# Kernel optimization log

Measured on AMD Instinct MI355X. Metric: run time of the kernel, lower is better.

Reference implementation:

```python
import jax, jax.numpy as jnp
import numpy as np

EPS = 1e-12

def _pairwise_dist(a, b):
    # a: [B,N,3], b: [B,M,3] -> Euclidean distances [B,N,M]
    d2 = (jnp.sum(a * a, -1)[:, :, None]
          + jnp.sum(b * b, -1)[:, None, :]
          - 2.0 * jnp.einsum('bnd,bmd->bnm', a, b))
    return jnp.sqrt(jnp.maximum(d2, EPS))


def setup_inputs() -> dict:
    key = jax.random.key(0)
    k1, k2, k3 = jax.random.split(key, 3)
    B, N, M = 16, 4096, 1024
    shape_xyz = jax.random.normal(k1, (B, N, 6), dtype=jnp.float32)
    skel_xyz = jax.random.normal(k2, (B, M, 3), dtype=jnp.float32)
    skel_nori = jax.random.normal(k3, (B, M, 3), dtype=jnp.float32)
    return {"shape_xyz": shape_xyz, "skel_xyz": skel_xyz, "skel_nori": skel_nori}


def reference(shape_xyz, skel_xyz, skel_nori):
    normal = shape_xyz[:, :, 3:6]          # [B,N,3]
    pts = shape_xyz[:, :, :3]              # [B,N,3]
    B = skel_nori.shape[0]

    # Chamfer-style closest distances (sum of min Euclidean distances, both ways)
    d_shape2skel = _pairwise_dist(pts, skel_xyz)   # [B,N,M]
    cd1 = jnp.sum(jnp.min(d_shape2skel, axis=2))
    cd2 = jnp.sum(jnp.min(d_shape2skel, axis=1))   # same matrix transposed
    loss_cd = (cd1 + cd2) * 0.0001

    # KNN (k=2) of each skeletal point among shape points (cKDTree equivalent)
    d_skel2shape = jnp.transpose(d_shape2skel, (0, 2, 1))  # [B,M,N]
    _, idx = jax.lax.top_k(-d_skel2shape, 2)               # [B,M,2]

    # Gather normals of the 2 nearest shape points: [B,M,2,3]
    knn_normals = jnp.take_along_axis(normal[:, None, :, :],
                                      idx[:, :, :, None], axis=2)
    dots = jnp.einsum('bmd,bmkd->bmk', skel_nori, knn_normals)  # [B,M,2]
    # |dot| averaged over k, summed over (b, j), divided by batch size
    loss_normal = jnp.sum(jnp.mean(jnp.abs(dots), axis=-1)) / B

    return loss_cd + 0.001 * loss_normal
```

## Files before the change

### kernel.cpp

```cpp
#include <hip/hip_runtime.h>
#include <cfloat>
#include <stdint.h>

#define B_ 16
#define N_ 4096
#define M_ 1024
#define EPS_ 1e-12f

__device__ __forceinline__ uint32_t umin3(uint32_t a, uint32_t b, uint32_t c) {
    return min(a, min(b, c));
}
__device__ __forceinline__ uint32_t umed3(uint32_t a, uint32_t b, uint32_t c) {
    return max(min(a, b), min(max(a, b), c));
}

__global__ __launch_bounds__(256, 6) void fused_kernel(const float* __restrict__ shape_xyz,
                                                       const float* __restrict__ skel_xyz,
                                                       const float* __restrict__ skel_nori,
                                                       float* __restrict__ out)
{
    __shared__ float4 ls4[1024];
    __shared__ float ws[4];

    const int tid = threadIdx.x;
    float v = 0.0f;

    if (blockIdx.x < 512) {
        const int id  = blockIdx.x;
        const int b   = id >> 5;
        const int sub = id & 31;

        const float4* g4 = (const float4*)(skel_xyz + (size_t)b * M_ * 3);
        const float4 r0 = g4[3 * tid + 0];
        const float4 r1 = g4[3 * tid + 1];
        const float4 r2 = g4[3 * tid + 2];

        const int sA = tid & 15;
        const int gA = tid >> 4;
        const int n0 = sub * 128 + gA * 8;
        const float* p = shape_xyz + ((size_t)b * N_ + n0) * 6;
        float m2x[8], m2y[8], m2z[8], pp[8], best[8];
#pragma unroll
        for (int k = 0; k < 8; ++k) {
            const float x = p[k * 6 + 0];
            const float y = p[k * 6 + 1];
            const float z = p[k * 6 + 2];
            m2x[k] = -2.0f * x; m2y[k] = -2.0f * y; m2z[k] = -2.0f * z;
            pp[k]  = fmaf(x, x, fmaf(y, y, z * z));
            best[k] = FLT_MAX;
        }

        {
            float x, y, z;
            x = r0.x; y = r0.y; z = r0.z;
            ls4[4 * tid + 0] = make_float4(x, y, z, fmaf(x, x, fmaf(y, y, z * z)));
            x = r0.w; y = r1.x; z = r1.y;
            ls4[4 * tid + 1] = make_float4(x, y, z, fmaf(x, x, fmaf(y, y, z * z)));
            x = r1.z; y = r1.w; z = r2.x;
            ls4[4 * tid + 2] = make_float4(x, y, z, fmaf(x, x, fmaf(y, y, z * z)));
            x = r2.y; y = r2.z; z = r2.w;
            ls4[4 * tid + 3] = make_float4(x, y, z, fmaf(x, x, fmaf(y, y, z * z)));
        }
        __syncthreads();

#pragma unroll 4
        for (int j = 0; j < 32; ++j) {
            const float4 s0 = ls4[j * 32 + sA];
            const float4 s1 = ls4[j * 32 + 16 + sA];
#pragma unroll
            for (int k = 0; k < 8; ++k) {
                const float t0 = fmaf(m2x[k], s0.x, fmaf(m2y[k], s0.y, fmaf(m2z[k], s0.z, s0.w)));
                const float t1 = fmaf(m2x[k], s1.x, fmaf(m2y[k], s1.y, fmaf(m2z[k], s1.z, s1.w)));
                best[k] = fminf(best[k], fminf(t0, t1));
            }
        }

#pragma unroll
        for (int off = 1; off < 16; off <<= 1) {
#pragma unroll
            for (int k = 0; k < 8; ++k) best[k] = fminf(best[k], __shfl_xor(best[k], off));
        }
        if (sA == 0) {
#pragma unroll
            for (int k = 0; k < 8; ++k) v += sqrtf(fmaxf(best[k] + pp[k], EPS_));
            v *= 1e-4f;
        }
    } else {
        const int id  = blockIdx.x - 512;
        const int b   = id >> 6;
        const int sub = id & 63;
        const int s   = tid & 31;
        const int g   = tid >> 5;
        const int m0  = sub * 16 + g * 2;

        float m2x[2], m2y[2], m2z[2], aa[2];
        uint32_t k1[2], k2[2];
        {
            const float* sq = skel_xyz + ((size_t)b * M_ + m0) * 3;
#pragma unroll
            for (int c = 0; c < 2; ++c) {
                const float x = sq[c * 3 + 0];
                const float y = sq[c * 3 + 1];
                const float z = sq[c * 3 + 2];
                m2x[c] = -2.0f * x; m2y[c] = -2.0f * y; m2z[c] = -2.0f * z;
                aa[c]  = fmaf(x, x, fmaf(y, y, z * z));
                k1[c] = 0xFFFFFFFFu; k2[c] = 0xFFFFFFFFu;
            }
        }

        const uint32_t HI = 0xFFFFF000u;
        const float* sb = shape_xyz + (size_t)b * N_ * 6;
        const float4* g4 = (const float4*)sb;

        float4 r[6];
#pragma unroll
        for (int k = 0; k < 6; ++k) r[k] = g4[6 * tid + k];

        for (int ph = 0; ph < 4; ++ph) {
            __syncthreads();
            {
                float x, y, z;
                x = r[0].x; y = r[0].y; z = r[0].z;
                ls4[4 * tid + 0] = make_float4(x, y, z, fmaf(x, x, fmaf(y, y, z * z)));
                x = r[1].z; y = r[1].w; z = r[2].x;
                ls4[4 * tid + 1] = make_float4(x, y, z, fmaf(x, x, fmaf(y, y, z * z)));
                x = r[3].x; y = r[3].y; z = r[3].z;
                ls4[4 * tid + 2] = make_float4(x, y, z, fmaf(x, x, fmaf(y, y, z * z)));
                x = r[4].z; y = r[4].w; z = r[5].x;
                ls4[4 * tid + 3] = make_float4(x, y, z, fmaf(x, x, fmaf(y, y, z * z)));
            }
            __syncthreads();
            if (ph < 3) {
#pragma unroll
                for (int k = 0; k < 6; ++k) r[k] = g4[(ph + 1) * 1536 + 6 * tid + k];
            }
            const uint32_t nb = (uint32_t)(ph * 1024);

#pragma unroll 4
            for (int j = 0; j < 16; ++j) {
                const float4 q0 = ls4[j * 64 + s];
                const float4 q1 = ls4[j * 64 + 32 + s];
                const uint32_t gn0 = nb + (uint32_t)(j * 64 + s);
                const uint32_t gn1 = gn0 + 32u;
#pragma unroll
                for (int c = 0; c < 2; ++c) {
                    const float t0 = fmaf(m2x[c], q0.x, fmaf(m2y[c], q0.y, fmaf(m2z[c], q0.z, q0.w + aa[c])));
                    const float t1 = fmaf(m2x[c], q1.x, fmaf(m2y[c], q1.y, fmaf(m2z[c], q1.z, q1.w + aa[c])));
                    const uint32_t kk0 = (__float_as_uint(t0) & HI) | gn0;
                    const uint32_t kk1 = (__float_as_uint(t1) & HI) | gn1;
                    k2[c] = min(k2[c], umed3(k1[c], kk0, kk1));
                    k1[c] = umin3(k1[c], kk0, kk1);
                }
            }
        }

#pragma unroll
        for (int off = 1; off < 32; off <<= 1) {
#pragma unroll
            for (int c = 0; c < 2; ++c) {
                const uint32_t o1 = (uint32_t)__shfl_xor((int)k1[c], off);
                const uint32_t o2 = (uint32_t)__shfl_xor((int)k2[c], off);
                const uint32_t nk2 = min(min(k2[c], o2), max(k1[c], o1));
                k1[c] = min(k1[c], o1);
                k2[c] = nk2;
            }
        }

        if (s == 0) {
            const float* no = skel_nori + ((size_t)b * M_ + m0) * 3;
            const float kN = 0.001f * 0.5f / (float)B_;
#pragma unroll
            for (int c = 0; c < 2; ++c) {
                const int i1 = (int)(k1[c] & 0xFFFu);
                const int i2 = (int)(k2[c] & 0xFFFu);
                const float* p1 = sb + (size_t)i1 * 6;
                const float* p2 = sb + (size_t)i2 * 6;
                const float ax = -0.5f * m2x[c], ay = -0.5f * m2y[c], az = -0.5f * m2z[c];
                const float dx = ax - p1[0], dy = ay - p1[1], dz = az - p1[2];
                const float d2 = fmaf(dx, dx, fmaf(dy, dy, dz * dz));
                const float q0 = no[c * 3 + 0], q1 = no[c * 3 + 1], q2 = no[c * 3 + 2];
                const float dot1 = q0 * p1[3] + q1 * p1[4] + q2 * p1[5];
                const float dot2 = q0 * p2[3] + q1 * p2[4] + q2 * p2[5];
                v += sqrtf(fmaxf(d2, EPS_)) * 1e-4f + (fabsf(dot1) + fabsf(dot2)) * kN;
            }
        }
    }

#pragma unroll
    for (int off = 32; off > 0; off >>= 1) v += __shfl_down(v, off);
    if ((tid & 63) == 0) ws[tid >> 6] = v;
    __syncthreads();
    if (tid == 0) atomicAdd(out, ws[0] + ws[1] + ws[2] + ws[3]);
}

extern "C" void kernel_launch(void* const* d_in, const int* in_sizes, int n_in,
                              void* d_out, int out_size, void* d_ws, size_t ws_size,
                              hipStream_t stream) {
    const float* shape_xyz = (const float*)d_in[0];
    const float* skel_xyz  = (const float*)d_in[1];
    const float* skel_nori = (const float*)d_in[2];
    float* out = (float*)d_out;

    hipMemsetAsync(out, 0, sizeof(float), stream);
    fused_kernel<<<1536, 256, 0, stream>>>(shape_xyz, skel_xyz, skel_nori, out);
}
```

Before: 87.46 us.

## Double per-thread register tiles in both chamfer and KNN halves, halve grid

Each thread in the shape-to-skeleton half now handles 16 points instead of 8. Each thread in the KNN half now handles 4 skeleton points instead of 2, staging 2048 shape points per phase in a doubled LDS buffer over 2 phases. Skeleton coordinates are pre-doubled when stored to LDS, so the inner loop negates the point instead of keeping precomputed -2x registers. The goal is more arithmetic per LDS load and fewer blocks, paid for with higher register pressure, lower occupancy (launch bounds 6 to 3, 768 blocks) and possible spills.

```diff
diff --git a/kernel.cpp b/kernel.cpp
--- a/kernel.cpp
+++ b/kernel.cpp
@@ -14,21 +14,20 @@
     return max(min(a, b), min(max(a, b), c));
 }
 
-__global__ __launch_bounds__(256, 6) void fused_kernel(const float* __restrict__ shape_xyz,
+__global__ __launch_bounds__(256, 3) void fused_kernel(const float* __restrict__ shape_xyz,
                                                        const float* __restrict__ skel_xyz,
                                                        const float* __restrict__ skel_nori,
                                                        float* __restrict__ out)
 {
-    __shared__ float4 ls4[1024];
+    __shared__ float4 ls4[2048];
     __shared__ float ws[4];
 
     const int tid = threadIdx.x;
     float v = 0.0f;
 
-    if (blockIdx.x < 512) {
-        const int id  = blockIdx.x;
-        const int b   = id >> 5;
-        const int sub = id & 31;
+    if (blockIdx.x < 256) {
+        const int b    = blockIdx.x >> 4;
+        const int tile = blockIdx.x & 15;
 
         const float4* g4 = (const float4*)(skel_xyz + (size_t)b * M_ * 3);
         const float4 r0 = g4[3 * tid + 0];
@@ -37,40 +36,39 @@
 
         const int sA = tid & 15;
         const int gA = tid >> 4;
-        const int n0 = sub * 128 + gA * 8;
+        const int n0 = tile * 256 + gA * 16;
         const float* p = shape_xyz + ((size_t)b * N_ + n0) * 6;
-        float m2x[8], m2y[8], m2z[8], pp[8], best[8];
-#pragma unroll
-        for (int k = 0; k < 8; ++k) {
-            const float x = p[k * 6 + 0];
-            const float y = p[k * 6 + 1];
-            const float z = p[k * 6 + 2];
-            m2x[k] = -2.0f * x; m2y[k] = -2.0f * y; m2z[k] = -2.0f * z;
-            pp[k]  = fmaf(x, x, fmaf(y, y, z * z));
+        float px[16], py[16], pz[16], pp[16], best[16];
+#pragma unroll
+        for (int k = 0; k < 16; ++k) {
+            px[k] = p[k * 6 + 0];
+            py[k] = p[k * 6 + 1];
+            pz[k] = p[k * 6 + 2];
+            pp[k] = fmaf(px[k], px[k], fmaf(py[k], py[k], pz[k] * pz[k]));
             best[k] = FLT_MAX;
         }
 
         {
             float x, y, z;
             x = r0.x; y = r0.y; z = r0.z;
-            ls4[4 * tid + 0] = make_float4(x, y, z, fmaf(x, x, fmaf(y, y, z * z)));
+            ls4[4 * tid + 0] = make_float4(2*x, 2*y, 2*z, fmaf(x, x, fmaf(y, y, z * z)));
             x = r0.w; y = r1.x; z = r1.y;
-            ls4[4 * tid + 1] = make_float4(x, y, z, fmaf(x, x, fmaf(y, y, z * z)));
+            ls4[4 * tid + 1] = make_float4(2*x, 2*y, 2*z, fmaf(x, x, fmaf(y, y, z * z)));
             x = r1.z; y = r1.w; z = r2.x;
-            ls4[4 * tid + 2] = make_float4(x, y, z, fmaf(x, x, fmaf(y, y, z * z)));
+            ls4[4 * tid + 2] = make_float4(2*x, 2*y, 2*z, fmaf(x, x, fmaf(y, y, z * z)));
             x = r2.y; y = r2.z; z = r2.w;
-            ls4[4 * tid + 3] = make_float4(x, y, z, fmaf(x, x, fmaf(y, y, z * z)));
+            ls4[4 * tid + 3] = make_float4(2*x, 2*y, 2*z, fmaf(x, x, fmaf(y, y, z * z)));
         }
         __syncthreads();
 
-#pragma unroll 4
+#pragma unroll 2
         for (int j = 0; j < 32; ++j) {
             const float4 s0 = ls4[j * 32 + sA];
             const float4 s1 = ls4[j * 32 + 16 + sA];
 #pragma unroll
-            for (int k = 0; k < 8; ++k) {
-                const float t0 = fmaf(m2x[k], s0.x, fmaf(m2y[k], s0.y, fmaf(m2z[k], s0.z, s0.w)));
-                const float t1 = fmaf(m2x[k], s1.x, fmaf(m2y[k], s1.y, fmaf(m2z[k], s1.z, s1.w)));
+            for (int k = 0; k < 16; ++k) {
+                const float t0 = fmaf(-px[k], s0.x, fmaf(-py[k], s0.y, fmaf(-pz[k], s0.z, s0.w)));
+                const float t1 = fmaf(-px[k], s1.x, fmaf(-py[k], s1.y, fmaf(-pz[k], s1.z, s1.w)));
                 best[k] = fminf(best[k], fminf(t0, t1));
             }
         }
@@ -78,27 +76,27 @@
 #pragma unroll
         for (int off = 1; off < 16; off <<= 1) {
 #pragma unroll
-            for (int k = 0; k < 8; ++k) best[k] = fminf(best[k], __shfl_xor(best[k], off));
+            for (int k = 0; k < 16; ++k) best[k] = fminf(best[k], __shfl_xor(best[k], off));
         }
         if (sA == 0) {
 #pragma unroll
-            for (int k = 0; k < 8; ++k) v += sqrtf(fmaxf(best[k] + pp[k], EPS_));
+            for (int k = 0; k < 16; ++k) v += sqrtf(fmaxf(best[k] + pp[k], EPS_));
             v *= 1e-4f;
         }
     } else {
-        const int id  = blockIdx.x - 512;
-        const int b   = id >> 6;
-        const int sub = id & 63;
+        const int id  = blockIdx.x - 256;
+        const int b   = id >> 5;
+        const int sub = id & 31;
         const int s   = tid & 31;
         const int g   = tid >> 5;
-        const int m0  = sub * 16 + g * 2;
-
-        float m2x[2], m2y[2], m2z[2], aa[2];
-        uint32_t k1[2], k2[2];
+        const int m0  = sub * 32 + g * 4;
+
+        float m2x[4], m2y[4], m2z[4], aa[4];
+        uint32_t k1[4], k2[4];
         {
             const float* sq = skel_xyz + ((size_t)b * M_ + m0) * 3;
 #pragma unroll
-            for (int c = 0; c < 2; ++c) {
+            for (int c = 0; c < 4; ++c) {
                 const float x = sq[c * 3 + 0];
                 const float y = sq[c * 3 + 1];
                 const float z = sq[c * 3 + 2];
@@ -112,38 +110,36 @@
         const float* sb = shape_xyz + (size_t)b * N_ * 6;
         const float4* g4 = (const float4*)sb;
 
-        float4 r[6];
-#pragma unroll
-        for (int k = 0; k < 6; ++k) r[k] = g4[6 * tid + k];
-
-        for (int ph = 0; ph < 4; ++ph) {
+        float4 r[12];
+#pragma unroll
+        for (int k = 0; k < 12; ++k) r[k] = g4[12 * tid + k];
+
+        for (int ph = 0; ph < 2; ++ph) {
             __syncthreads();
-            {
+#pragma unroll
+            for (int i = 0; i < 4; ++i) {
                 float x, y, z;
-                x = r[0].x; y = r[0].y; z = r[0].z;
-                ls4[4 * tid + 0] = make_float4(x, y, z, fmaf(x, x, fmaf(y, y, z * z)));
-                x = r[1].z; y = r[1].w; z = r[2].x;
-                ls4[4 * tid + 1] = make_float4(x, y, z, fmaf(x, x, fmaf(y, y, z * z)));
-                x = r[3].x; y = r[3].y; z = r[3].z;
-                ls4[4 * tid + 2] = make_float4(x, y, z, fmaf(x, x, fmaf(y, y, z * z)));
-                x = r[4].z; y = r[4].w; z = r[5].x;
-                ls4[4 * tid + 3] = make_float4(x, y, z, fmaf(x, x, fmaf(y, y, z * z)));
+                x = r[3 * i].x; y = r[3 * i].y; z = r[3 * i].z;
+                ls4[8 * tid + 2 * i + 0] = make_float4(x, y, z, fmaf(x, x, fmaf(y, y, z * z)));
+                x = r[3 * i + 1].z; y = r[3 * i + 1].w; z = r[3 * i + 2].x;
+                ls4[8 * tid + 2 * i + 1] = make_float4(x, y, z, fmaf(x, x, fmaf(y, y, z * z)));
             }
             __syncthreads();
-            if (ph < 3) {
-#pragma unroll
-                for (int k = 0; k < 6; ++k) r[k] = g4[(ph + 1) * 1536 + 6 * tid + k];
-            }
-            const uint32_t nb = (uint32_t)(ph * 1024);
+            if (ph == 0) {
+#pragma unroll
+                for (int k = 0; k < 12; ++k) r[k] = g4[3072 + 12 * tid + k];
+            }
+            const uint32_t nb = (uint32_t)(ph * 2048);
 
 #pragma unroll 4
-            for (int j = 0; j < 16; ++j) {
-                const float4 q0 = ls4[j * 64 + s];
-                const float4 q1 = ls4[j * 64 + 32 + s];
-                const uint32_t gn0 = nb + (uint32_t)(j * 64 + s);
+            for (int j = 0; j < 32; ++j) {
+                const int nl = j * 64 + s;
+                const float4 q0 = ls4[nl];
+                const float4 q1 = ls4[nl + 32];
+                const uint32_t gn0 = nb + (uint32_t)nl;
                 const uint32_t gn1 = gn0 + 32u;
 #pragma unroll
-                for (int c = 0; c < 2; ++c) {
+                for (int c = 0; c < 4; ++c) {
                     const float t0 = fmaf(m2x[c], q0.x, fmaf(m2y[c], q0.y, fmaf(m2z[c], q0.z, q0.w + aa[c])));
                     const float t1 = fmaf(m2x[c], q1.x, fmaf(m2y[c], q1.y, fmaf(m2z[c], q1.z, q1.w + aa[c])));
                     const uint32_t kk0 = (__float_as_uint(t0) & HI) | gn0;
@@ -157,7 +153,7 @@
 #pragma unroll
         for (int off = 1; off < 32; off <<= 1) {
 #pragma unroll
-            for (int c = 0; c < 2; ++c) {
+            for (int c = 0; c < 4; ++c) {
                 const uint32_t o1 = (uint32_t)__shfl_xor((int)k1[c], off);
                 const uint32_t o2 = (uint32_t)__shfl_xor((int)k2[c], off);
                 const uint32_t nk2 = min(min(k2[c], o2), max(k1[c], o1));
@@ -170,7 +166,7 @@
             const float* no = skel_nori + ((size_t)b * M_ + m0) * 3;
             const float kN = 0.001f * 0.5f / (float)B_;
 #pragma unroll
-            for (int c = 0; c < 2; ++c) {
+            for (int c = 0; c < 4; ++c) {
                 const int i1 = (int)(k1[c] & 0xFFFu);
                 const int i2 = (int)(k2[c] & 0xFFFu);
                 const float* p1 = sb + (size_t)i1 * 6;
@@ -202,5 +198,5 @@
     float* out = (float*)d_out;
 
     hipMemsetAsync(out, 0, sizeof(float), stream);
-    fused_kernel<<<1536, 256, 0, stream>>>(shape_xyz, skel_xyz, skel_nori, out);
-}
+    fused_kernel<<<768, 256, 0, stream>>>(shape_xyz, skel_xyz, skel_nori, out);
+}
```

New measurement: 85.35 us. -2.4%, faster.
